# Kernel tuning notes

Measured on AMD Instinct MI355X. Metric: run time of the kernel, lower is better.

Reference implementation:

```python
import jax, jax.numpy as jnp
import numpy as np

H, W = 512, 512          # image_shape
FH, FW = 64, 64          # filter_size
NUM_PARTS = 256
N = 8192                 # number of placed parts


def setup_inputs() -> dict:
    key = jax.random.key(0)
    k1, k2, k3, k4 = jax.random.split(key, 4)
    filters = jax.random.normal(k1, (NUM_PARTS, FH, FW), dtype=jnp.float32)
    part = jax.random.randint(k2, (N,), 0, NUM_PARTS)
    row = jax.random.randint(k3, (N,), 0, H)
    col = jax.random.randint(k4, (N,), 0, W)
    phw_list = jnp.stack([part, row, col], axis=1).astype(jnp.int32)  # [N,3]
    return {"phw_list": phw_list, "filters": filters}


def reference(phw_list, filters):
    # Original: for each part i, slice filters[part_idx] to the in-bounds window
    # and += into canvas[from_r:to_r, from_c:to_c].
    # Equivalent vectorized form: scatter-add FULL filters onto a padded canvas
    # (pad = full filter size on each side, so all writes are in-bounds), then
    # crop back to (H, W). Clipping via crop == the original's slice clipping.
    fo_h, fo_w = FH // 2, FW // 2  # filter center offsets
    part = phw_list[:, 0]
    row = phw_list[:, 1]
    col = phw_list[:, 2]

    filts = filters[part]                                  # (N, FH, FW) gather
    r0 = row - fo_h + FH                                   # top-left row in padded canvas
    c0 = col - fo_w + FW                                   # top-left col in padded canvas
    rr = r0[:, None, None] + jnp.arange(FH)[None, :, None]  # (N, FH, 1)
    cc = c0[:, None, None] + jnp.arange(FW)[None, None, :]  # (N, 1, FW)

    padded = jnp.zeros((H + 2 * FH, W + 2 * FW), dtype=filters.dtype)
    padded = padded.at[rr, cc].add(filts)                  # overlapping scatter-add
    return padded[FH:FH + H, FW:FW + W]                    # (H, W) canvas
```

## Files before the change

### kernel.cpp

```cpp
#include <hip/hip_runtime.h>


#define H_  512
#define W_  512
#define FH_ 64
#define FW_ 64
#define TILE_ 32
#define THREADS_ 256
#define SEG_LEN_ 1024

__device__ __forceinline__ int clamp63(int v) {
    return min(max(v, 0), 63);
}

__global__ __launch_bounds__(THREADS_, 8)
void render_tile_kernel(const int* __restrict__ phw,
                        const float* __restrict__ filters,
                        float* __restrict__ out, int n) {
    __shared__ unsigned int s_list[SEG_LEN_];
    __shared__ int s_cnt;

    const int t   = threadIdx.x;
    const int tx0 = blockIdx.x * TILE_;
    const int ty0 = blockIdx.y * TILE_;
    const int k0  = blockIdx.z * SEG_LEN_;
    const int k1  = (k0 + SEG_LEN_ < n) ? (k0 + SEG_LEN_) : n;

    if (t == 0) s_cnt = 0;
    __syncthreads();

    for (int k = k0 + t; k < k1; k += THREADS_) {
        const int part = phw[k * 3 + 0];
        const int row  = phw[k * 3 + 1];
        const int col  = phw[k * 3 + 2];
        const bool hit =
            (row >= ty0 - (FH_ / 2 - 1)) && (row <= ty0 + TILE_ - 1 + FH_ / 2) &&
            (col >= tx0 - (FW_ / 2 - 1)) && (col <= tx0 + TILE_ - 1 + FW_ / 2);
        if (hit) {
            const int idx = atomicAdd(&s_cnt, 1);
            s_list[idx] = ((unsigned)part << 18) | ((unsigned)row << 9) | (unsigned)col;
        }
    }
    __syncthreads();
    const int cnt = s_cnt;

    const int xl    = t & 31;
    const int yb    = t >> 5;
    const int x     = tx0 + xl;
    const int ybase = ty0 + yb;

    float acc0 = 0.f, acc1 = 0.f, acc2 = 0.f, acc3 = 0.f;

    auto body = [&](unsigned v) {
        const int part = (int)__builtin_amdgcn_readfirstlane(v >> 18);
        const int row  = (int)__builtin_amdgcn_readfirstlane((v >> 9) & 511u);
        const int col  = (int)__builtin_amdgcn_readfirstlane(v & 511u);
        const float* __restrict__ f = filters + (part << 12);

        const int  j   = x - col + (FW_ / 2);
        const int  jc  = clamp63(j);
        const bool jok = (unsigned)j < (unsigned)FW_;
        const int  i0  = ybase - row + (FH_ / 2);

        const int ia = i0;      const int ib = i0 + 8;
        const int ic = i0 + 16; const int id = i0 + 24;
        const float va = f[clamp63(ia) * FW_ + jc];
        const float vb = f[clamp63(ib) * FW_ + jc];
        const float vc = f[clamp63(ic) * FW_ + jc];
        const float vd = f[clamp63(id) * FW_ + jc];
        acc0 += (jok && (unsigned)ia < (unsigned)FH_) ? va : 0.f;
        acc1 += (jok && (unsigned)ib < (unsigned)FH_) ? vb : 0.f;
        acc2 += (jok && (unsigned)ic < (unsigned)FH_) ? vc : 0.f;
        acc3 += (jok && (unsigned)id < (unsigned)FH_) ? vd : 0.f;
    };

    int k = 0;
    for (; k + 4 <= cnt; k += 4) {
        const uint4 vv = *(const uint4*)&s_list[k];
        body(vv.x); body(vv.y); body(vv.z); body(vv.w);
    }
    for (; k < cnt; ++k) body(s_list[k]);

    atomicAdd(&out[(ybase +  0) * W_ + x], acc0);
    atomicAdd(&out[(ybase +  8) * W_ + x], acc1);
    atomicAdd(&out[(ybase + 16) * W_ + x], acc2);
    atomicAdd(&out[(ybase + 24) * W_ + x], acc3);
}

extern "C" void kernel_launch(void* const* d_in, const int* in_sizes, int n_in,
                              void* d_out, int out_size, void* d_ws, size_t ws_size,
                              hipStream_t stream) {
    const int*   phw     = (const int*)d_in[0];
    const float* filters = (const float*)d_in[1];
    float*       out     = (float*)d_out;
    const int n = in_sizes[0] / 3;

    hipMemsetAsync(out, 0, (size_t)H_ * W_ * sizeof(float), stream);

    const int segs = (n + SEG_LEN_ - 1) / SEG_LEN_;
    dim3 grid(W_ / TILE_, H_ / TILE_, segs);
    render_tile_kernel<<<grid, THREADS_, 0, stream>>>(phw, filters, out, n);
}
```

Measured before the change: 81.62 us.

## Write per-segment partial planes and reduce them instead of atomic adds

Each segment block now stores its accumulators into a private plane in the workspace with plain stores, and a separate vectorized kernel sums the planes into the output. This removes the memset and the global float atomics. In exchange it adds a kernel launch and extra global traffic (8 planes of 1 MB each, written and then read). The code falls back to the atomic path when the workspace is too small.

Result: no change. 82.60 us (+1.2%).

```diff
diff --git a/kernel.cpp b/kernel.cpp
--- a/kernel.cpp
+++ b/kernel.cpp
@@ -8,15 +8,18 @@
 #define TILE_ 32
 #define THREADS_ 256
 #define SEG_LEN_ 1024
+#define PLANE_   (H_ * W_)
 
 __device__ __forceinline__ int clamp63(int v) {
     return min(max(v, 0), 63);
 }
 
+template<bool PLANES>
 __global__ __launch_bounds__(THREADS_, 8)
 void render_tile_kernel(const int* __restrict__ phw,
                         const float* __restrict__ filters,
-                        float* __restrict__ out, int n) {
+                        float* __restrict__ dst,
+                        int n) {
     __shared__ unsigned int s_list[SEG_LEN_];
     __shared__ int s_cnt;
 
@@ -81,10 +84,43 @@
     }
     for (; k < cnt; ++k) body(s_list[k]);
 
-    atomicAdd(&out[(ybase +  0) * W_ + x], acc0);
-    atomicAdd(&out[(ybase +  8) * W_ + x], acc1);
-    atomicAdd(&out[(ybase + 16) * W_ + x], acc2);
-    atomicAdd(&out[(ybase + 24) * W_ + x], acc3);
+    if constexpr (PLANES) {
+        float* __restrict__ plane = dst + (size_t)blockIdx.z * PLANE_;
+        plane[(ybase +  0) * W_ + x] = acc0;
+        plane[(ybase +  8) * W_ + x] = acc1;
+        plane[(ybase + 16) * W_ + x] = acc2;
+        plane[(ybase + 24) * W_ + x] = acc3;
+    } else {
+        atomicAdd(&dst[(ybase +  0) * W_ + x], acc0);
+        atomicAdd(&dst[(ybase +  8) * W_ + x], acc1);
+        atomicAdd(&dst[(ybase + 16) * W_ + x], acc2);
+        atomicAdd(&dst[(ybase + 24) * W_ + x], acc3);
+    }
+}
+
+template<int SEGS>
+__global__ __launch_bounds__(256)
+void reduce_planes_fixed(const float* __restrict__ planes, float* __restrict__ out) {
+    const int i = (blockIdx.x * 256 + threadIdx.x) * 4;
+    float4 a = *(const float4*)&planes[i];
+#pragma unroll
+    for (int s = 1; s < SEGS; ++s) {
+        const float4 b = *(const float4*)&planes[(size_t)s * PLANE_ + i];
+        a.x += b.x; a.y += b.y; a.z += b.z; a.w += b.w;
+    }
+    *(float4*)&out[i] = a;
+}
+
+__global__ __launch_bounds__(256)
+void reduce_planes_var(const float* __restrict__ planes, float* __restrict__ out,
+                       int segs) {
+    const int i = (blockIdx.x * 256 + threadIdx.x) * 4;
+    float4 a = *(const float4*)&planes[i];
+    for (int s = 1; s < segs; ++s) {
+        const float4 b = *(const float4*)&planes[(size_t)s * PLANE_ + i];
+        a.x += b.x; a.y += b.y; a.z += b.z; a.w += b.w;
+    }
+    *(float4*)&out[i] = a;
 }
 
 extern "C" void kernel_launch(void* const* d_in, const int* in_sizes, int n_in,
@@ -95,9 +131,28 @@
     float*       out     = (float*)d_out;
     const int n = in_sizes[0] / 3;
 
-    hipMemsetAsync(out, 0, (size_t)H_ * W_ * sizeof(float), stream);
+    if (n <= 0) {
+        hipMemsetAsync(out, 0, (size_t)H_ * W_ * sizeof(float), stream);
+        return;
+    }
 
     const int segs = (n + SEG_LEN_ - 1) / SEG_LEN_;
+    const size_t plane_bytes = (size_t)segs * PLANE_ * sizeof(float);
     dim3 grid(W_ / TILE_, H_ / TILE_, segs);
-    render_tile_kernel<<<grid, THREADS_, 0, stream>>>(phw, filters, out, n);
+
+    if (d_ws != nullptr && ws_size >= plane_bytes) {
+        float* planes = (float*)d_ws;
+        render_tile_kernel<true><<<grid, dim3(THREADS_), 0, stream>>>(
+            phw, filters, planes, n);
+        const int rblocks = PLANE_ / 4 / 256;
+        if (segs == 8) {
+            reduce_planes_fixed<8><<<dim3(rblocks), dim3(256), 0, stream>>>(planes, out);
+        } else {
+            reduce_planes_var<<<dim3(rblocks), dim3(256), 0, stream>>>(planes, out, segs);
+        }
+    } else {
+        hipMemsetAsync(out, 0, (size_t)H_ * W_ * sizeof(float), stream);
+        render_tile_kernel<false><<<grid, dim3(THREADS_), 0, stream>>>(
+            phw, filters, out, n);
+    }
 }
```
